# Performance work log

Hardware: AMD Instinct MI355X
Metric: run time of the kernel (lower is better)

Reference implementation:

```python
import jax, jax.numpy as jnp
import numpy as np

G = 5   # grid intervals
K = 5   # spline order
H = 2.0 / G  # knot spacing on [-1, 1]
# Extended uniform knot vector: G + 2K + 1 = 16 knots from -1-K*H to 1+K*H.
KNOTS = jnp.arange(-K, G + K + 1, dtype=jnp.float32) * H - 1.0  # (16,)


def bspline_bases(x):
    """Cox-de Boor B-spline bases. x: (B, in) -> (B, in, G+K)."""
    g = KNOTS[None, :]            # (1, 16), broadcasts over (B, in, .)
    xe = x[..., None]             # (B, in, 1)
    # degree-0 indicator bases: (B, in, G+2K)
    b = ((xe >= g[:, :-1]) & (xe < g[:, 1:])).astype(x.dtype)
    for d in range(1, K + 1):
        left = (xe - g[:, : -(d + 1)]) / (g[:, d:-1] - g[:, : -(d + 1)]) * b[..., :-1]
        right = (g[:, d + 1 :] - xe) / (g[:, d + 1 :] - g[:, 1:-d]) * b[..., 1:]
        b = left + right
    return b  # (B, in, G+K)


def kan_layer(x, Wb, Ws):
    # residual base path: silu(x) @ Wb  (in,out)
    # spline path: sum_i sum_k B[b,i,k] * Ws[i,o,k]
    bases = bspline_bases(x)
    return jax.nn.silu(x) @ Wb + jnp.einsum('bik,iok->bo', bases, Ws)


def setup_inputs() -> dict:
    key = jax.random.key(0)
    ks = jax.random.split(key, 7)
    B, IN, OUT, NB = 16384, 1024, 64, G + K
    s = 0.1  # small init scale
    return {
        'x':   jax.random.uniform(ks[0], (B, IN), dtype=jnp.float32),
        'Wb1': jax.random.normal(ks[1], (IN, 5), dtype=jnp.float32) * s,
        'Ws1': jax.random.normal(ks[2], (IN, 5, NB), dtype=jnp.float32) * s,
        'Wb2': jax.random.normal(ks[3], (5, 5), dtype=jnp.float32) * s,
        'Ws2': jax.random.normal(ks[4], (5, 5, NB), dtype=jnp.float32) * s,
        'Wb3': jax.random.normal(ks[5], (5, OUT), dtype=jnp.float32) * s,
        'Ws3': jax.random.normal(ks[6], (5, OUT, NB), dtype=jnp.float32) * s,
    }


def reference(x, Wb1, Ws1, Wb2, Ws2, Wb3, Ws3):
    h = kan_layer(x, Wb1, Ws1)   # (B, 5)
    h = kan_layer(h, Wb2, Ws2)   # (B, 5)
    h = kan_layer(h, Wb3, Ws3)   # (B, 64)
    return jax.nn.softmax(h, axis=-1)
```

## Files before the change

### kernel.cpp

```cpp
#include <hip/hip_runtime.h>
#include <cstdint>
#include <cstddef>


#define NROWS 16384
#define IN1   1024
#define WPACK 48
#define NCHUNK 8
#define RGROUPS (NROWS / 64)

__global__ void k0_pack(const float* __restrict__ Wb1, const float* __restrict__ Ws1,
                        float* __restrict__ w1p) {
  int e = blockIdx.x * 256 + threadIdx.x;
  if (e >= IN1 * WPACK) return;
  int i = e / WPACK;
  int c = e - i * WPACK;
  float v = 0.0f;
  if (c < 40) {
    int o = c >> 3, k = (c & 7) + 2;
    v = Ws1[(i * 5 + o) * 10 + k];
  } else if (c < 45) {
    v = Wb1[i * 5 + (c - 40)];
  }
  w1p[e] = v;
}

#define C120(a) ((a) / 120.0f)

__device__ __forceinline__ void kan1_elem(float x, const float* __restrict__ w,
                                          float& a0, float& a1, float& a2,
                                          float& a3, float& a4) {
  float v  = fmaf(x, 2.5f, 7.5f);
  float u  = __builtin_amdgcn_fractf(v);
  float N0 = fmaf(fmaf(fmaf(fmaf(fmaf(C120(-1.f), u, C120(5.f)),  u, C120(-10.f)), u, C120(10.f)),  u, C120(-5.f)),  u, C120(1.f));
  float N1 = fmaf(fmaf(fmaf(fmaf(fmaf(C120(5.f),  u, C120(-20.f)), u, C120(20.f)),  u, C120(20.f)),  u, C120(-50.f)), u, C120(26.f));
  float N2 = fmaf(fmaf(fmaf(fmaf(fmaf(C120(-10.f),u, C120(30.f)),  u, C120(0.f)),   u, C120(-60.f)), u, C120(0.f)),   u, C120(66.f));
  float N3 = fmaf(fmaf(fmaf(fmaf(fmaf(C120(10.f), u, C120(-20.f)), u, C120(-20.f)), u, C120(20.f)),  u, C120(50.f)),  u, C120(26.f));
  float N4 = fmaf(fmaf(fmaf(fmaf(fmaf(C120(-5.f), u, C120(5.f)),   u, C120(10.f)),  u, C120(10.f)),  u, C120(5.f)),   u, C120(1.f));
  float u2 = u * u;
  float N5 = u2 * u2 * u * C120(1.f);
  bool e0 = v < 8.0f;
  bool e2 = v >= 9.0f;
  float B0 = e0 ? N0 : 0.0f;
  float B1 = e0 ? N1 : (e2 ? 0.0f : N0);
  float B2 = e0 ? N2 : (e2 ? N0 : N1);
  float B3 = e0 ? N3 : (e2 ? N1 : N2);
  float B4 = e0 ? N4 : (e2 ? N2 : N3);
  float B5v= e0 ? N5 : (e2 ? N3 : N4);
  float B6 = e0 ? 0.0f : (e2 ? N4 : N5);
  float B7 = e2 ? N5 : 0.0f;
  float si = x * __builtin_amdgcn_rcpf(1.0f + __expf(-x));
  a0 = fmaf(si, w[40], a0);
  a0 = fmaf(B0, w[0], a0); a0 = fmaf(B1, w[1], a0); a0 = fmaf(B2, w[2], a0); a0 = fmaf(B3, w[3], a0);
  a0 = fmaf(B4, w[4], a0); a0 = fmaf(B5v, w[5], a0); a0 = fmaf(B6, w[6], a0); a0 = fmaf(B7, w[7], a0);
  a1 = fmaf(si, w[41], a1);
  a1 = fmaf(B0, w[8], a1); a1 = fmaf(B1, w[9], a1); a1 = fmaf(B2, w[10], a1); a1 = fmaf(B3, w[11], a1);
  a1 = fmaf(B4, w[12], a1); a1 = fmaf(B5v, w[13], a1); a1 = fmaf(B6, w[14], a1); a1 = fmaf(B7, w[15], a1);
  a2 = fmaf(si, w[42], a2);
  a2 = fmaf(B0, w[16], a2); a2 = fmaf(B1, w[17], a2); a2 = fmaf(B2, w[18], a2); a2 = fmaf(B3, w[19], a2);
  a2 = fmaf(B4, w[20], a2); a2 = fmaf(B5v, w[21], a2); a2 = fmaf(B6, w[22], a2); a2 = fmaf(B7, w[23], a2);
  a3 = fmaf(si, w[43], a3);
  a3 = fmaf(B0, w[24], a3); a3 = fmaf(B1, w[25], a3); a3 = fmaf(B2, w[26], a3); a3 = fmaf(B3, w[27], a3);
  a3 = fmaf(B4, w[28], a3); a3 = fmaf(B5v, w[29], a3); a3 = fmaf(B6, w[30], a3); a3 = fmaf(B7, w[31], a3);
  a4 = fmaf(si, w[44], a4);
  a4 = fmaf(B0, w[32], a4); a4 = fmaf(B1, w[33], a4); a4 = fmaf(B2, w[34], a4); a4 = fmaf(B3, w[35], a4);
  a4 = fmaf(B4, w[36], a4); a4 = fmaf(B5v, w[37], a4); a4 = fmaf(B6, w[38], a4); a4 = fmaf(B7, w[39], a4);
}

__global__ __launch_bounds__(256, 4) void k1_layer1(const float* __restrict__ x,
                                                    const float* __restrict__ w1p,
                                                    float* __restrict__ hp) {
  __shared__ float part[4 * 320];
  int tid  = threadIdx.x;
  int wv   = tid >> 6, lane = tid & 63;
  int bid  = blockIdx.x;
  int rg   = bid >> 3, c = bid & 7;
  int wvu  = __builtin_amdgcn_readfirstlane(wv);
  int i0   = c * 128 + wvu * 32;
  const float* xp = x + (size_t)(rg * 64 + lane) * IN1 + i0;
  const float* wb = w1p + (size_t)i0 * WPACK;
  float a0 = 0.f, a1 = 0.f, a2 = 0.f, a3 = 0.f, a4 = 0.f;
#pragma unroll 2
  for (int s = 0; s < 8; ++s) {
    float4 xv = reinterpret_cast<const float4*>(xp)[s];
    const float* w = wb + (size_t)s * 4 * WPACK;
    kan1_elem(xv.x, w,             a0, a1, a2, a3, a4);
    kan1_elem(xv.y, w + WPACK,     a0, a1, a2, a3, a4);
    kan1_elem(xv.z, w + 2 * WPACK, a0, a1, a2, a3, a4);
    kan1_elem(xv.w, w + 3 * WPACK, a0, a1, a2, a3, a4);
  }
  float* pr = part + wv * 320 + lane * 5;
  pr[0] = a0; pr[1] = a1; pr[2] = a2; pr[3] = a3; pr[4] = a4;
  __syncthreads();
  for (int t = tid; t < 320; t += 256) {
    int row = t & 63, o = t >> 6;
    float s = part[row * 5 + o] + part[320 + row * 5 + o] +
              part[640 + row * 5 + o] + part[960 + row * 5 + o];
    hp[(size_t)bid * 320 + t] = s;
  }
}

__device__ __forceinline__ void bases10(float xv, float* bb) {
  float v = fmaf(xv, 2.5f, 7.5f);
  float b[15];
#pragma unroll
  for (int j = 0; j < 15; ++j)
    b[j] = (v >= (float)j && v < (float)(j + 1)) ? 1.0f : 0.0f;
#pragma unroll
  for (int d = 1; d <= 5; ++d) {
    const float inv = 1.0f / (float)d;
#pragma unroll
    for (int j = 0; j + d < 15; ++j) {
      float left  = (v - (float)j) * inv;
      float right = ((float)(j + d + 1) - v) * inv;
      b[j] = left * b[j] + right * b[j + 1];
    }
  }
#pragma unroll
  for (int k = 0; k < 10; ++k) bb[k] = b[k];
}

__global__ __launch_bounds__(256) void k2_tail(const float* __restrict__ hp,
                        const float* __restrict__ Wb2, const float* __restrict__ Ws2,
                        const float* __restrict__ Wb3, const float* __restrict__ Ws3,
                        float* __restrict__ out) {
  __shared__ float lsi1[16 * 5];
  __shared__ float lb1 [16 * 55];
  __shared__ float lsi2[16 * 5];
  __shared__ float lb2 [16 * 55];
  __shared__ float llog[16 * 65];
  __shared__ float lred[16 * 16];
  __shared__ float lmx [16];
  __shared__ float linv[16];
  int tid  = threadIdx.x;
  int bg   = blockIdx.x;
  int rg64 = bg >> 2;
  int sub  = (bg & 3) * 16;

  if (tid < 80) {
    int row = tid & 15, i = tid >> 4;
    float s = 0.f;
#pragma unroll
    for (int c = 0; c < NCHUNK; ++c)
      s += hp[(size_t)(rg64 * NCHUNK + c) * 320 + i * 64 + sub + row];
    lsi1[row * 5 + i] = s / (1.0f + __expf(-s));
    float bb[10];
    bases10(s, bb);
#pragma unroll
    for (int k = 0; k < 10; ++k) lb1[row * 55 + i * 11 + k] = bb[k];
  }
  __syncthreads();

  if (tid < 80) {
    int row = tid & 15, o = tid >> 4;
    float acc = 0.f;
#pragma unroll
    for (int i = 0; i < 5; ++i) {
      acc = fmaf(lsi1[row * 5 + i], Wb2[i * 5 + o], acc);
#pragma unroll
      for (int k = 0; k < 10; ++k)
        acc = fmaf(lb1[row * 55 + i * 11 + k], Ws2[(i * 5 + o) * 10 + k], acc);
    }
    lsi2[row * 5 + o] = acc / (1.0f + __expf(-acc));
    float bb[10];
    bases10(acc, bb);
#pragma unroll
    for (int k = 0; k < 10; ++k) lb2[row * 55 + o * 11 + k] = bb[k];
  }
  __syncthreads();

  {
    int o  = tid & 63;
    int r0 = (tid >> 6) * 4;
    float lg[4] = {0.f, 0.f, 0.f, 0.f};
#pragma unroll
    for (int i = 0; i < 5; ++i) {
      float wbv = Wb3[i * 64 + o];
      float w[10];
#pragma unroll
      for (int k = 0; k < 10; ++k) w[k] = Ws3[(i * 64 + o) * 10 + k];
#pragma unroll
      for (int rr = 0; rr < 4; ++rr) {
        int row = r0 + rr;
        lg[rr] = fmaf(lsi2[row * 5 + i], wbv, lg[rr]);
#pragma unroll
        for (int k = 0; k < 10; ++k)
          lg[rr] = fmaf(lb2[row * 55 + i * 11 + k], w[k], lg[rr]);
      }
    }
#pragma unroll
    for (int rr = 0; rr < 4; ++rr) llog[(r0 + rr) * 65 + o] = lg[rr];
  }
  __syncthreads();

  int q = tid >> 4, row = tid & 15;
  {
    float m = -1e30f;
#pragma unroll
    for (int oo = 0; oo < 4; ++oo)
      m = fmaxf(m, llog[row * 65 + q * 4 + oo]);
    lred[q * 16 + row] = m;
  }
  __syncthreads();
  if (tid < 16) {
    float m = -1e30f;
#pragma unroll
    for (int k = 0; k < 16; ++k) m = fmaxf(m, lred[k * 16 + tid]);
    lmx[tid] = m;
  }
  __syncthreads();
  {
    float m = lmx[row];
    float s = 0.f;
#pragma unroll
    for (int oo = 0; oo < 4; ++oo) {
      int idx = row * 65 + q * 4 + oo;
      float e = __expf(llog[idx] - m);
      llog[idx] = e;
      s += e;
    }
    lred[q * 16 + row] = s;
  }
  __syncthreads();
  if (tid < 16) {
    float s = 0.f;
#pragma unroll
    for (int k = 0; k < 16; ++k) s += lred[k * 16 + tid];
    linv[tid] = 1.0f / s;
  }
  __syncthreads();
#pragma unroll
  for (int uu = 0; uu < 4; ++uu) {
    int u = tid + uu * 256;
    int r = u >> 6, o = u & 63;
    out[(size_t)(bg * 16 + r) * 64 + o] = llog[r * 65 + o] * linv[r];
  }
}

extern "C" void kernel_launch(void* const* d_in, const int* in_sizes, int n_in,
                              void* d_out, int out_size, void* d_ws, size_t ws_size,
                              hipStream_t stream) {
  const float* x   = (const float*)d_in[0];
  const float* Wb1 = (const float*)d_in[1];
  const float* Ws1 = (const float*)d_in[2];
  const float* Wb2 = (const float*)d_in[3];
  const float* Ws2 = (const float*)d_in[4];
  const float* Wb3 = (const float*)d_in[5];
  const float* Ws3 = (const float*)d_in[6];
  float* out = (float*)d_out;

  float* w1p = (float*)d_ws;
  float* hp  = w1p + (size_t)IN1 * WPACK;

  hipLaunchKernelGGL(k0_pack, dim3((IN1 * WPACK) / 256), dim3(256), 0, stream,
                     Wb1, Ws1, w1p);
  hipLaunchKernelGGL(k1_layer1, dim3(RGROUPS * NCHUNK), dim3(256), 0, stream,
                     x, w1p, hp);
  hipLaunchKernelGGL(k2_tail, dim3(NROWS / 16), dim3(256), 0, stream,
                     hp, Wb2, Ws2, Wb3, Ws3, out);
}
```

Baseline: 148.3 us.

## Fuse layer-1 with tail and map lanes to features for coalesced loads

Restructures layer 1 so lanes span input features and each wave processes 8 rows, holding per-lane packed weights in registers and reusing them across rows. Partial sums are reduced by wave shuffles and shared memory, and the layer-2/3/softmax tail runs in the same kernel, removing the intermediate workspace round trip and one launch. Weights are repacked into float4-interleaved groups to match. It adds heavy register pressure and shuffle reductions, which could cause spills or reduce occupancy.

Result: slower. 159.4 us (+7.5%).

```diff
diff --git a/kernel.cpp b/kernel.cpp
--- a/kernel.cpp
+++ b/kernel.cpp
@@ -5,29 +5,25 @@
 
 #define NROWS 16384
 #define IN1   1024
-#define WPACK 48
-#define NCHUNK 8
-#define RGROUPS (NROWS / 64)
 
 __global__ void k0_pack(const float* __restrict__ Wb1, const float* __restrict__ Ws1,
-                        float* __restrict__ w1p) {
+                        float* __restrict__ w4) {
   int e = blockIdx.x * 256 + threadIdx.x;
-  if (e >= IN1 * WPACK) return;
-  int i = e / WPACK;
-  int c = e - i * WPACK;
+  int g = e >> 12, rem = e & 4095, i = rem >> 2, c = rem & 3;
+  int slot = g * 4 + c;
   float v = 0.0f;
-  if (c < 40) {
-    int o = c >> 3, k = (c & 7) + 2;
+  if (slot < 40) {
+    int o = slot >> 3, k = (slot & 7) + 2;
     v = Ws1[(i * 5 + o) * 10 + k];
-  } else if (c < 45) {
-    v = Wb1[i * 5 + (c - 40)];
-  }
-  w1p[e] = v;
+  } else if (slot < 45) {
+    v = Wb1[i * 5 + (slot - 40)];
+  }
+  w4[(size_t)g * 4096 + i * 4 + c] = v;
 }
 
 #define C120(a) ((a) / 120.0f)
 
-__device__ __forceinline__ void kan1_elem(float x, const float* __restrict__ w,
+__device__ __forceinline__ void kan1_elem(float x, const float (&w)[48],
                                           float& a0, float& a1, float& a2,
                                           float& a3, float& a4) {
   float v  = fmaf(x, 2.5f, 7.5f);
@@ -67,39 +63,6 @@
   a4 = fmaf(B4, w[36], a4); a4 = fmaf(B5v, w[37], a4); a4 = fmaf(B6, w[38], a4); a4 = fmaf(B7, w[39], a4);
 }
 
-__global__ __launch_bounds__(256, 4) void k1_layer1(const float* __restrict__ x,
-                                                    const float* __restrict__ w1p,
-                                                    float* __restrict__ hp) {
-  __shared__ float part[4 * 320];
-  int tid  = threadIdx.x;
-  int wv   = tid >> 6, lane = tid & 63;
-  int bid  = blockIdx.x;
-  int rg   = bid >> 3, c = bid & 7;
-  int wvu  = __builtin_amdgcn_readfirstlane(wv);
-  int i0   = c * 128 + wvu * 32;
-  const float* xp = x + (size_t)(rg * 64 + lane) * IN1 + i0;
-  const float* wb = w1p + (size_t)i0 * WPACK;
-  float a0 = 0.f, a1 = 0.f, a2 = 0.f, a3 = 0.f, a4 = 0.f;
-#pragma unroll 2
-  for (int s = 0; s < 8; ++s) {
-    float4 xv = reinterpret_cast<const float4*>(xp)[s];
-    const float* w = wb + (size_t)s * 4 * WPACK;
-    kan1_elem(xv.x, w,             a0, a1, a2, a3, a4);
-    kan1_elem(xv.y, w + WPACK,     a0, a1, a2, a3, a4);
-    kan1_elem(xv.z, w + 2 * WPACK, a0, a1, a2, a3, a4);
-    kan1_elem(xv.w, w + 3 * WPACK, a0, a1, a2, a3, a4);
-  }
-  float* pr = part + wv * 320 + lane * 5;
-  pr[0] = a0; pr[1] = a1; pr[2] = a2; pr[3] = a3; pr[4] = a4;
-  __syncthreads();
-  for (int t = tid; t < 320; t += 256) {
-    int row = t & 63, o = t >> 6;
-    float s = part[row * 5 + o] + part[320 + row * 5 + o] +
-              part[640 + row * 5 + o] + part[960 + row * 5 + o];
-    hp[(size_t)bid * 320 + t] = s;
-  }
-}
-
 __device__ __forceinline__ void bases10(float xv, float* bb) {
   float v = fmaf(xv, 2.5f, 7.5f);
   float b[15];
@@ -120,10 +83,12 @@
   for (int k = 0; k < 10; ++k) bb[k] = b[k];
 }
 
-__global__ __launch_bounds__(256) void k2_tail(const float* __restrict__ hp,
-                        const float* __restrict__ Wb2, const float* __restrict__ Ws2,
-                        const float* __restrict__ Wb3, const float* __restrict__ Ws3,
-                        float* __restrict__ out) {
+__global__ __launch_bounds__(256, 4) void k1_fused(
+    const float* __restrict__ x, const float* __restrict__ w4,
+    const float* __restrict__ Wb2, const float* __restrict__ Ws2,
+    const float* __restrict__ Wb3, const float* __restrict__ Ws3,
+    float* __restrict__ out) {
+  __shared__ float part[4][40];
   __shared__ float lsi1[16 * 5];
   __shared__ float lb1 [16 * 55];
   __shared__ float lsi2[16 * 5];
@@ -132,17 +97,61 @@
   __shared__ float lred[16 * 16];
   __shared__ float lmx [16];
   __shared__ float linv[16];
+
   int tid  = threadIdx.x;
-  int bg   = blockIdx.x;
-  int rg64 = bg >> 2;
-  int sub  = (bg & 3) * 16;
+  int wv   = tid >> 6, lane = tid & 63;
+  int b    = blockIdx.x;
+  int h    = wv & 1;
+  int rtl  = wv >> 1;
+  int row0 = b * 16 + rtl * 8;
+
+  const float*  xb = x + (size_t)row0 * IN1 + h * 512 + lane;
+  const float4* wp = (const float4*)w4 + h * 512 + lane;
+
+  float acc[8][5];
+#pragma unroll
+  for (int r = 0; r < 8; ++r)
+#pragma unroll
+    for (int o = 0; o < 5; ++o) acc[r][o] = 0.0f;
+
+  for (int s = 0; s < 8; ++s) {
+    const float4* wps = wp + s * 64;
+    float wr[48];
+#pragma unroll
+    for (int g = 0; g < 12; ++g) {
+      float4 q = wps[(size_t)g * 1024];
+      wr[4*g] = q.x; wr[4*g+1] = q.y; wr[4*g+2] = q.z; wr[4*g+3] = q.w;
+    }
+    const float* xs = xb + s * 64;
+    float xv[8];
+#pragma unroll
+    for (int r = 0; r < 8; ++r) xv[r] = xs[(size_t)r * IN1];
+#pragma unroll
+    for (int r = 0; r < 8; ++r)
+      kan1_elem(xv[r], wr, acc[r][0], acc[r][1], acc[r][2], acc[r][3], acc[r][4]);
+  }
+
+#pragma unroll
+  for (int r = 0; r < 8; ++r)
+#pragma unroll
+    for (int o = 0; o < 5; ++o) {
+      float v = acc[r][o];
+#pragma unroll
+      for (int m = 1; m < 64; m <<= 1) v += __shfl_xor(v, m);
+      acc[r][o] = v;
+    }
+  if (lane == 0) {
+#pragma unroll
+    for (int r = 0; r < 8; ++r)
+#pragma unroll
+      for (int o = 0; o < 5; ++o) part[wv][r * 5 + o] = acc[r][o];
+  }
+  __syncthreads();
 
   if (tid < 80) {
     int row = tid & 15, i = tid >> 4;
-    float s = 0.f;
-#pragma unroll
-    for (int c = 0; c < NCHUNK; ++c)
-      s += hp[(size_t)(rg64 * NCHUNK + c) * 320 + i * 64 + sub + row];
+    int wA = (row >> 3) * 2;
+    float s = part[wA][(row & 7) * 5 + i] + part[wA + 1][(row & 7) * 5 + i];
     lsi1[row * 5 + i] = s / (1.0f + __expf(-s));
     float bb[10];
     bases10(s, bb);
@@ -153,17 +162,17 @@
 
   if (tid < 80) {
     int row = tid & 15, o = tid >> 4;
-    float acc = 0.f;
+    float a = 0.f;
 #pragma unroll
     for (int i = 0; i < 5; ++i) {
-      acc = fmaf(lsi1[row * 5 + i], Wb2[i * 5 + o], acc);
+      a = fmaf(lsi1[row * 5 + i], Wb2[i * 5 + o], a);
 #pragma unroll
       for (int k = 0; k < 10; ++k)
-        acc = fmaf(lb1[row * 55 + i * 11 + k], Ws2[(i * 5 + o) * 10 + k], acc);
-    }
-    lsi2[row * 5 + o] = acc / (1.0f + __expf(-acc));
+        a = fmaf(lb1[row * 55 + i * 11 + k], Ws2[(i * 5 + o) * 10 + k], a);
+    }
+    lsi2[row * 5 + o] = a / (1.0f + __expf(-a));
     float bb[10];
-    bases10(acc, bb);
+    bases10(a, bb);
 #pragma unroll
     for (int k = 0; k < 10; ++k) lb2[row * 55 + o * 11 + k] = bb[k];
   }
@@ -233,7 +242,7 @@
   for (int uu = 0; uu < 4; ++uu) {
     int u = tid + uu * 256;
     int r = u >> 6, o = u & 63;
-    out[(size_t)(bg * 16 + r) * 64 + o] = llog[r * 65 + o] * linv[r];
+    out[(size_t)(b * 16 + r) * 64 + o] = llog[r * 65 + o] * linv[r];
   }
 }
 
@@ -249,13 +258,9 @@
   const float* Ws3 = (const float*)d_in[6];
   float* out = (float*)d_out;
 
-  float* w1p = (float*)d_ws;
-  float* hp  = w1p + (size_t)IN1 * WPACK;
-
-  hipLaunchKernelGGL(k0_pack, dim3((IN1 * WPACK) / 256), dim3(256), 0, stream,
-                     Wb1, Ws1, w1p);
-  hipLaunchKernelGGL(k1_layer1, dim3(RGROUPS * NCHUNK), dim3(256), 0, stream,
-                     x, w1p, hp);
-  hipLaunchKernelGGL(k2_tail, dim3(NROWS / 16), dim3(256), 0, stream,
-                     hp, Wb2, Ws2, Wb3, Ws3, out);
-}
+  float* w4 = (float*)d_ws;
+
+  hipLaunchKernelGGL(k0_pack, dim3(192), dim3(256), 0, stream, Wb1, Ws1, w4);
+  hipLaunchKernelGGL(k1_fused, dim3(NROWS / 16), dim3(256), 0, stream,
+                     x, w4, Wb2, Ws2, Wb3, Ws3, out);
+}
```
